# Optimization experiments

Measured on AMD Instinct MI355X. Metric: run time of the kernel, lower is better.

Reference implementation:

```python
import jax, jax.numpy as jnp
import numpy as np

E = 320000   # num edges / messages
N = 10000    # num target nodes (dim_size)
C = 256      # in_channels == out_channels


def setup_inputs() -> dict:
    key = jax.random.key(0)
    k1, k2, k3, k4, k5, k6 = jax.random.split(key, 6)
    s = 1.0 / np.sqrt(C)  # torch Linear default init bound
    return {
        "from_tensor": jax.random.normal(k1, (E, C), dtype=jnp.float32),
        "to_index": jax.random.randint(k2, (E,), 0, N),
        "dim_size": N,
        "W1": jax.random.uniform(k3, (C, C), jnp.float32, -s, s),
        "b1": jax.random.uniform(k4, (C,), jnp.float32, -s, s),
        "W2": jax.random.uniform(k5, (C, C), jnp.float32, -s, s),
        "b2": jax.random.uniform(k6, (C,), jnp.float32, -s, s),
    }


def reference(from_tensor, to_index, dim_size, W1, b1, W2, b2):
    # InterMessage with transform_scatter=True, num_layers=2, reduction='mean':
    # message = MLP(from_tensor); out = scatter_mean(message, to_index, dim_size)
    m = jax.nn.relu(from_tensor @ W1 + b1)          # [E, C]
    m = jax.nn.relu(m @ W2 + b2)                    # [E, C]
    sums = jax.ops.segment_sum(m, to_index, num_segments=dim_size)  # [N, C]
    cnt = jax.ops.segment_sum(jnp.ones((m.shape[0], 1), m.dtype), to_index,
                              num_segments=dim_size)                # [N, 1]
    # scatter-mean: empty segments produce 0 (matches torch_scatter 'mean')
    return jnp.where(cnt > 0, sums / jnp.maximum(cnt, 1.0), 0.0)
```

## Files before the change

### kernel.cpp

```cpp
#include <hip/hip_runtime.h>

#define NUM_E 320000
#define NUM_N 10000
#define PADC 32

typedef __attribute__((ext_vector_type(8))) short bf16x8;
typedef __attribute__((ext_vector_type(4))) float f32x4;

__device__ __forceinline__ short f2bf(float f) {
  unsigned u = __builtin_bit_cast(unsigned, f);
  u += 0x7FFFu + ((u >> 16) & 1u);
  return (short)(u >> 16);
}

__device__ __forceinline__ unsigned pack2bf(float x, float y) {
  unsigned ux = __builtin_bit_cast(unsigned, x);
  unsigned uy = __builtin_bit_cast(unsigned, y);
  ux += 0x7FFFu + ((ux >> 16) & 1u);
  uy += 0x7FFFu + ((uy >> 16) & 1u);
  return __builtin_amdgcn_perm(uy, ux, 0x07060302u);
}

__global__ __launch_bounds__(256) void zero_repack_k(
    const float* __restrict__ W1, const float* __restrict__ W2,
    short* __restrict__ Wp, int* __restrict__ cntA, int* __restrict__ cursor,
    float* __restrict__ out) {
  const int gtid = blockIdx.x * 256 + threadIdx.x;
  const int gsz = gridDim.x * 256;
  if (gtid == 0) *cursor = 0;
  for (int i = gtid; i < 640000; i += gsz)
    reinterpret_cast<float4*>(out)[i] = make_float4(0.f, 0.f, 0.f, 0.f);
  for (int i = gtid; i < NUM_N * PADC / 4; i += gsz)
    reinterpret_cast<int4*>(cntA)[i] = make_int4(0, 0, 0, 0);
  if (gtid < 16384) {
    const float* W = (gtid & 8192) ? W2 : W1;
    int r = gtid & 8191;
    short* dst = Wp + (gtid >> 13) * 65536 + r * 8;
    int j = r >> 9;
    int s = (r >> 6) & 7;
    int lane = r & 63;
    int n = j * 16 + (lane & 15);
    int k0 = s * 32 + (lane >> 4) * 8;
    short tmp[8];
#pragma unroll
    for (int e = 0; e < 8; ++e) tmp[e] = f2bf(W[(k0 + e) * 256 + n]);
#pragma unroll
    for (int e = 0; e < 8; ++e) dst[e] = tmp[e];
  }
}

__global__ __launch_bounds__(256) void hist_k(const int* __restrict__ idx,
                                              int* __restrict__ cntA) {
  int e = blockIdx.x * 256 + threadIdx.x;
  if (e < NUM_E) atomicAdd(&cntA[idx[e] * PADC], 1);
}

__global__ __launch_bounds__(256) void alloc_k(const int* __restrict__ cntA,
                                               int* __restrict__ fillP,
                                               float* __restrict__ inv,
                                               int* __restrict__ cursor) {
  int n = blockIdx.x * 256 + threadIdx.x;
  int lane = threadIdx.x & 63;
  int c = (n < NUM_N) ? cntA[n * PADC] : 0;
  int pre = c;
#pragma unroll
  for (int off = 1; off < 64; off <<= 1) {
    int v = __shfl_up(pre, off, 64);
    if (lane >= off) pre += v;
  }
  int tot = __shfl(pre, 63, 64);
  int base = 0;
  if (lane == 63) base = atomicAdd(cursor, tot);
  base = __shfl(base, 63, 64);
  if (n < NUM_N) {
    fillP[n * PADC] = base + pre - c;
    inv[n] = (c > 0) ? 1.0f / (float)c : 0.0f;
  }
}

__global__ __launch_bounds__(256) void scatter_k(const int* __restrict__ idx,
                                                 int* __restrict__ fillP,
                                                 int* __restrict__ sorted) {
  int e = blockIdx.x * 256 + threadIdx.x;
  if (e < NUM_E) {
    int ix = idx[e];
    int pos = atomicAdd(&fillP[ix * PADC], 1);
    sorted[pos] = e;
  }
}

__global__ __launch_bounds__(256, 3) void fused_mlp_gather(
    const float* __restrict__ X, const int* __restrict__ idx,
    const int* __restrict__ sorted,
    const short* __restrict__ Wp1, const short* __restrict__ Wp2,
    const float* __restrict__ b1, const float* __restrict__ b2,
    const float* __restrict__ inv, float* __restrict__ out) {
  __shared__ __align__(16) short Xl[64][264];
  __shared__ int idxl[64];
  __shared__ int se[64];
  __shared__ int segLo[64];
  __shared__ int segN[64];
  __shared__ int nsegS;

  const int tid = threadIdx.x;
  const int wave = tid >> 6;
  const int lane = tid & 63;
  const int q = lane >> 4;
  const int m = lane & 15;
  const int row0 = blockIdx.x * 64;

  if (tid < 64) {
    int e = sorted[row0 + tid];
    se[tid] = e;
    idxl[tid] = idx[e];
  }
  __syncthreads();

  float4 vbuf[16];
#pragma unroll
  for (int k = 0; k < 16; ++k) {
    int i = tid + k * 256;
    int r = i >> 6, c4 = i & 63;
    vbuf[k] = reinterpret_cast<const float4*>(X + (size_t)se[r] * 256)[c4];
  }
#pragma unroll
  for (int k = 0; k < 16; ++k) {
    int i = tid + k * 256;
    int r = i >> 6, c4 = i & 63;
    uint2 p;
    p.x = pack2bf(vbuf[k].x, vbuf[k].y);
    p.y = pack2bf(vbuf[k].z, vbuf[k].w);
    *reinterpret_cast<uint2*>(&Xl[r][c4 * 4]) = p;
  }
  __syncthreads();

  if (wave == 0) {
    bool flag = (lane == 0) || (idxl[lane] != idxl[lane - 1]);
    unsigned long long mask = __ballot(flag);
    if (lane == 0) nsegS = (int)__popcll(mask);
    if (flag) {
      int sidx = (int)__popcll(mask & ((1ull << lane) - 1ull));
      segLo[sidx] = lane;
      segN[sidx] = idxl[lane];
    }
  }

  f32x4 acc[4][4];
#pragma unroll
  for (int mi = 0; mi < 4; ++mi)
#pragma unroll
    for (int nj = 0; nj < 4; ++nj) acc[mi][nj] = (f32x4)0.0f;

#pragma unroll
  for (int s = 0; s < 8; ++s) {
    bf16x8 a[4], b[4];
#pragma unroll
    for (int mi = 0; mi < 4; ++mi)
      a[mi] = *reinterpret_cast<const bf16x8*>(&Xl[mi * 16 + m][s * 32 + q * 8]);
#pragma unroll
    for (int nj = 0; nj < 4; ++nj)
      b[nj] = *reinterpret_cast<const bf16x8*>(
          Wp1 + (size_t)(((wave * 4 + nj) * 8 + s) * 64 + lane) * 8);
    __builtin_amdgcn_s_setprio(1);
#pragma unroll
    for (int mi = 0; mi < 4; ++mi)
#pragma unroll
      for (int nj = 0; nj < 4; ++nj)
        acc[mi][nj] = __builtin_amdgcn_mfma_f32_16x16x32_bf16(a[mi], b[nj],
                                                              acc[mi][nj], 0, 0, 0);
    __builtin_amdgcn_s_setprio(0);
  }
  __syncthreads();

  float bias1[4];
#pragma unroll
  for (int nj = 0; nj < 4; ++nj) bias1[nj] = b1[wave * 64 + nj * 16 + m];
#pragma unroll
  for (int mi = 0; mi < 4; ++mi)
#pragma unroll
    for (int nj = 0; nj < 4; ++nj)
#pragma unroll
      for (int r4 = 0; r4 < 4; ++r4) {
        float v = fmaxf(acc[mi][nj][r4] + bias1[nj], 0.0f);
        Xl[mi * 16 + q * 4 + r4][wave * 64 + nj * 16 + m] = f2bf(v);
      }
  __syncthreads();

#pragma unroll
  for (int mi = 0; mi < 4; ++mi)
#pragma unroll
    for (int nj = 0; nj < 4; ++nj) acc[mi][nj] = (f32x4)0.0f;

#pragma unroll
  for (int s = 0; s < 8; ++s) {
    bf16x8 a[4], b[4];
#pragma unroll
    for (int mi = 0; mi < 4; ++mi)
      a[mi] = *reinterpret_cast<const bf16x8*>(&Xl[mi * 16 + m][s * 32 + q * 8]);
#pragma unroll
    for (int nj = 0; nj < 4; ++nj)
      b[nj] = *reinterpret_cast<const bf16x8*>(
          Wp2 + (size_t)(((wave * 4 + nj) * 8 + s) * 64 + lane) * 8);
    __builtin_amdgcn_s_setprio(1);
#pragma unroll
    for (int mi = 0; mi < 4; ++mi)
#pragma unroll
      for (int nj = 0; nj < 4; ++nj)
        acc[mi][nj] = __builtin_amdgcn_mfma_f32_16x16x32_bf16(a[mi], b[nj],
                                                              acc[mi][nj], 0, 0, 0);
    __builtin_amdgcn_s_setprio(0);
  }

  float bias2[4];
#pragma unroll
  for (int nj = 0; nj < 4; ++nj) bias2[nj] = b2[wave * 64 + nj * 16 + m];
#pragma unroll
  for (int mi = 0; mi < 4; ++mi)
#pragma unroll
    for (int nj = 0; nj < 4; ++nj)
#pragma unroll
      for (int r4 = 0; r4 < 4; ++r4)
        acc[mi][nj][r4] = fmaxf(acc[mi][nj][r4] + bias2[nj], 0.0f);

  int nseg = nsegS;
  for (int s = 0; s < nseg; ++s) {
    int lo = segLo[s];
    int hi = (s + 1 < nseg) ? segLo[s + 1] : 64;
    int node = segN[s];
    float sum[4] = {0.0f, 0.0f, 0.0f, 0.0f};
#pragma unroll
    for (int mi = 0; mi < 4; ++mi)
#pragma unroll
      for (int r4 = 0; r4 < 4; ++r4) {
        int row = mi * 16 + q * 4 + r4;
        float msk = (row >= lo && row < hi) ? 1.0f : 0.0f;
#pragma unroll
        for (int nj = 0; nj < 4; ++nj) sum[nj] = fmaf(msk, acc[mi][nj][r4], sum[nj]);
      }
    float scale = inv[node];
#pragma unroll
    for (int nj = 0; nj < 4; ++nj) {
      float v = sum[nj];
      v += __shfl_xor(v, 16, 64);
      v += __shfl_xor(v, 32, 64);
      if (q == 0 && v != 0.0f)
        atomicAdd(&out[(size_t)node * 256 + wave * 64 + nj * 16 + m], v * scale);
    }
  }
}

extern "C" void kernel_launch(void* const* d_in, const int* in_sizes, int n_in,
                              void* d_out, int out_size, void* d_ws, size_t ws_size,
                              hipStream_t stream) {
  const float* X   = (const float*)d_in[0];
  const int*   idx = (const int*)d_in[1];
  const float* W1  = (const float*)d_in[3];
  const float* b1  = (const float*)d_in[4];
  const float* W2  = (const float*)d_in[5];
  const float* b2  = (const float*)d_in[6];
  float* out = (float*)d_out;

  char* ws = (char*)d_ws;
  short* Wp     = (short*)(ws);
  int*   cntA   = (int*)(ws + 262144);
  int*   fillP  = (int*)(ws + 1542144);
  float* inv    = (float*)(ws + 2822144);
  int*   cursor = (int*)(ws + 2863104);
  int*   sorted = cntA;

  zero_repack_k<<<2048, 256, 0, stream>>>(W1, W2, Wp, cntA, cursor, out);
  hist_k<<<(NUM_E + 255) / 256, 256, 0, stream>>>(idx, cntA);
  alloc_k<<<40, 256, 0, stream>>>(cntA, fillP, inv, cursor);
  scatter_k<<<(NUM_E + 255) / 256, 256, 0, stream>>>(idx, fillP, sorted);
  fused_mlp_gather<<<NUM_E / 64, 256, 0, stream>>>(
      X, idx, sorted, Wp, Wp + 65536, b1, b2, inv, out);
}
```

Before: 545.3 us.

## Software-pipeline gather of next edge tile behind MLP compute in persistent blocks

```diff
diff --git a/kernel.cpp b/kernel.cpp
--- a/kernel.cpp
+++ b/kernel.cpp
@@ -89,162 +89,199 @@
   }
 }
 
-__global__ __launch_bounds__(256, 3) void fused_mlp_gather(
+__global__ __launch_bounds__(256, 2) void fused_mlp_gather(
     const float* __restrict__ X, const int* __restrict__ idx,
     const int* __restrict__ sorted,
     const short* __restrict__ Wp1, const short* __restrict__ Wp2,
     const float* __restrict__ b1, const float* __restrict__ b2,
     const float* __restrict__ inv, float* __restrict__ out) {
-  __shared__ __align__(16) short Xl[64][264];
-  __shared__ int idxl[64];
-  __shared__ int se[64];
-  __shared__ int segLo[64];
-  __shared__ int segN[64];
-  __shared__ int nsegS;
+  __shared__ __align__(16) short Xl[2][64][264];
+  __shared__ int segLo[2][64];
+  __shared__ int segN[2][64];
+  __shared__ int nsegS[2];
 
   const int tid = threadIdx.x;
   const int wave = tid >> 6;
   const int lane = tid & 63;
   const int q = lane >> 4;
   const int m = lane & 15;
-  const int row0 = blockIdx.x * 64;
-
-  if (tid < 64) {
-    int e = sorted[row0 + tid];
-    se[tid] = e;
-    idxl[tid] = idx[e];
-  }
-  __syncthreads();
+  const int row0 = blockIdx.x * 256;
+
+  float bias1v[4], bias2v[4];
+#pragma unroll
+  for (int nj = 0; nj < 4; ++nj) {
+    bias1v[nj] = b1[wave * 64 + nj * 16 + m];
+    bias2v[nj] = b2[wave * 64 + nj * 16 + m];
+  }
 
   float4 vbuf[16];
-#pragma unroll
-  for (int k = 0; k < 16; ++k) {
-    int i = tid + k * 256;
-    int r = i >> 6, c4 = i & 63;
-    vbuf[k] = reinterpret_cast<const float4*>(X + (size_t)se[r] * 256)[c4];
-  }
-#pragma unroll
-  for (int k = 0; k < 16; ++k) {
-    int i = tid + k * 256;
-    int r = i >> 6, c4 = i & 63;
-    uint2 p;
-    p.x = pack2bf(vbuf[k].x, vbuf[k].y);
-    p.y = pack2bf(vbuf[k].z, vbuf[k].w);
-    *reinterpret_cast<uint2*>(&Xl[r][c4 * 4]) = p;
-  }
-  __syncthreads();
-
-  if (wave == 0) {
-    bool flag = (lane == 0) || (idxl[lane] != idxl[lane - 1]);
-    unsigned long long mask = __ballot(flag);
-    if (lane == 0) nsegS = (int)__popcll(mask);
-    if (flag) {
-      int sidx = (int)__popcll(mask & ((1ull << lane) - 1ull));
-      segLo[sidx] = lane;
-      segN[sidx] = idxl[lane];
-    }
-  }
-
-  f32x4 acc[4][4];
-#pragma unroll
-  for (int mi = 0; mi < 4; ++mi)
-#pragma unroll
-    for (int nj = 0; nj < 4; ++nj) acc[mi][nj] = (f32x4)0.0f;
-
-#pragma unroll
-  for (int s = 0; s < 8; ++s) {
-    bf16x8 a[4], b[4];
+
+  {
+    int ew = sorted[row0 + lane];
+    if (wave == 0) {
+      int ix = idx[ew];
+      int prev = __shfl_up(ix, 1, 64);
+      bool flag = (lane == 0) || (ix != prev);
+      unsigned long long mask = __ballot(flag);
+      if (lane == 0) nsegS[0] = (int)__popcll(mask);
+      if (flag) {
+        int sidx = (int)__popcll(mask & ((1ull << lane) - 1ull));
+        segLo[0][sidx] = lane;
+        segN[0][sidx] = ix;
+      }
+    }
+#pragma unroll
+    for (int k = 0; k < 16; ++k) {
+      int e = __shfl(ew, k * 4 + wave, 64);
+      vbuf[k] = reinterpret_cast<const float4*>(X + (size_t)e * 256)[lane];
+    }
+#pragma unroll
+    for (int k = 0; k < 16; ++k) {
+      uint2 pk;
+      pk.x = pack2bf(vbuf[k].x, vbuf[k].y);
+      pk.y = pack2bf(vbuf[k].z, vbuf[k].w);
+      *reinterpret_cast<uint2*>(&Xl[0][k * 4 + wave][lane * 4]) = pk;
+    }
+  }
+
+  for (int t = 0; t < 4; ++t) {
+    const int p = t & 1;
+
+    bool sflag = false;
+    int ssidx = 0, six = 0, snseg = 0;
+    if (t < 3) {
+      int ew = sorted[row0 + (t + 1) * 64 + lane];
+      if (wave == 0) {
+        int ix = idx[ew];
+        int prev = __shfl_up(ix, 1, 64);
+        sflag = (lane == 0) || (ix != prev);
+        unsigned long long mask = __ballot(sflag);
+        snseg = (int)__popcll(mask);
+        ssidx = (int)__popcll(mask & ((1ull << lane) - 1ull));
+        six = ix;
+      }
+#pragma unroll
+      for (int k = 0; k < 16; ++k) {
+        int e = __shfl(ew, k * 4 + wave, 64);
+        vbuf[k] = reinterpret_cast<const float4*>(X + (size_t)e * 256)[lane];
+      }
+      __builtin_amdgcn_sched_barrier(0);
+    }
+    __syncthreads();
+
+    if (t < 3 && wave == 0) {
+      if (lane == 0) nsegS[1 - p] = snseg;
+      if (sflag) {
+        segLo[1 - p][ssidx] = lane;
+        segN[1 - p][ssidx] = six;
+      }
+    }
+
+    f32x4 acc[4][4];
 #pragma unroll
     for (int mi = 0; mi < 4; ++mi)
-      a[mi] = *reinterpret_cast<const bf16x8*>(&Xl[mi * 16 + m][s * 32 + q * 8]);
-#pragma unroll
-    for (int nj = 0; nj < 4; ++nj)
-      b[nj] = *reinterpret_cast<const bf16x8*>(
-          Wp1 + (size_t)(((wave * 4 + nj) * 8 + s) * 64 + lane) * 8);
-    __builtin_amdgcn_s_setprio(1);
+#pragma unroll
+      for (int nj = 0; nj < 4; ++nj) acc[mi][nj] = (f32x4)0.0f;
+
+#pragma unroll
+    for (int s = 0; s < 8; ++s) {
+      bf16x8 a[4], b[4];
+#pragma unroll
+      for (int mi = 0; mi < 4; ++mi)
+        a[mi] = *reinterpret_cast<const bf16x8*>(&Xl[p][mi * 16 + m][s * 32 + q * 8]);
+#pragma unroll
+      for (int nj = 0; nj < 4; ++nj)
+        b[nj] = *reinterpret_cast<const bf16x8*>(
+            Wp1 + (size_t)(((wave * 4 + nj) * 8 + s) * 64 + lane) * 8);
+      __builtin_amdgcn_s_setprio(1);
+#pragma unroll
+      for (int mi = 0; mi < 4; ++mi)
+#pragma unroll
+        for (int nj = 0; nj < 4; ++nj)
+          acc[mi][nj] = __builtin_amdgcn_mfma_f32_16x16x32_bf16(a[mi], b[nj],
+                                                                acc[mi][nj], 0, 0, 0);
+      __builtin_amdgcn_s_setprio(0);
+    }
+    __syncthreads();
+
 #pragma unroll
     for (int mi = 0; mi < 4; ++mi)
 #pragma unroll
       for (int nj = 0; nj < 4; ++nj)
-        acc[mi][nj] = __builtin_amdgcn_mfma_f32_16x16x32_bf16(a[mi], b[nj],
-                                                              acc[mi][nj], 0, 0, 0);
-    __builtin_amdgcn_s_setprio(0);
-  }
-  __syncthreads();
-
-  float bias1[4];
-#pragma unroll
-  for (int nj = 0; nj < 4; ++nj) bias1[nj] = b1[wave * 64 + nj * 16 + m];
-#pragma unroll
-  for (int mi = 0; mi < 4; ++mi)
-#pragma unroll
-    for (int nj = 0; nj < 4; ++nj)
-#pragma unroll
-      for (int r4 = 0; r4 < 4; ++r4) {
-        float v = fmaxf(acc[mi][nj][r4] + bias1[nj], 0.0f);
-        Xl[mi * 16 + q * 4 + r4][wave * 64 + nj * 16 + m] = f2bf(v);
-      }
-  __syncthreads();
-
-#pragma unroll
-  for (int mi = 0; mi < 4; ++mi)
-#pragma unroll
-    for (int nj = 0; nj < 4; ++nj) acc[mi][nj] = (f32x4)0.0f;
-
-#pragma unroll
-  for (int s = 0; s < 8; ++s) {
-    bf16x8 a[4], b[4];
+#pragma unroll
+        for (int r4 = 0; r4 < 4; ++r4) {
+          float v = fmaxf(acc[mi][nj][r4] + bias1v[nj], 0.0f);
+          Xl[p][mi * 16 + q * 4 + r4][wave * 64 + nj * 16 + m] = f2bf(v);
+        }
+    __syncthreads();
+
 #pragma unroll
     for (int mi = 0; mi < 4; ++mi)
-      a[mi] = *reinterpret_cast<const bf16x8*>(&Xl[mi * 16 + m][s * 32 + q * 8]);
-#pragma unroll
-    for (int nj = 0; nj < 4; ++nj)
-      b[nj] = *reinterpret_cast<const bf16x8*>(
-          Wp2 + (size_t)(((wave * 4 + nj) * 8 + s) * 64 + lane) * 8);
-    __builtin_amdgcn_s_setprio(1);
+#pragma unroll
+      for (int nj = 0; nj < 4; ++nj) acc[mi][nj] = (f32x4)0.0f;
+
+#pragma unroll
+    for (int s = 0; s < 8; ++s) {
+      bf16x8 a[4], b[4];
+#pragma unroll
+      for (int mi = 0; mi < 4; ++mi)
+        a[mi] = *reinterpret_cast<const bf16x8*>(&Xl[p][mi * 16 + m][s * 32 + q * 8]);
+#pragma unroll
+      for (int nj = 0; nj < 4; ++nj)
+        b[nj] = *reinterpret_cast<const bf16x8*>(
+            Wp2 + (size_t)(((wave * 4 + nj) * 8 + s) * 64 + lane) * 8);
+      __builtin_amdgcn_s_setprio(1);
+#pragma unroll
+      for (int mi = 0; mi < 4; ++mi)
+#pragma unroll
+        for (int nj = 0; nj < 4; ++nj)
+          acc[mi][nj] = __builtin_amdgcn_mfma_f32_16x16x32_bf16(a[mi], b[nj],
+                                                                acc[mi][nj], 0, 0, 0);
+      __builtin_amdgcn_s_setprio(0);
+    }
+
 #pragma unroll
     for (int mi = 0; mi < 4; ++mi)
 #pragma unroll
       for (int nj = 0; nj < 4; ++nj)
-        acc[mi][nj] = __builtin_amdgcn_mfma_f32_16x16x32_bf16(a[mi], b[nj],
-                                                              acc[mi][nj], 0, 0, 0);
-    __builtin_amdgcn_s_setprio(0);
-  }
-
-  float bias2[4];
-#pragma unroll
-  for (int nj = 0; nj < 4; ++nj) bias2[nj] = b2[wave * 64 + nj * 16 + m];
-#pragma unroll
-  for (int mi = 0; mi < 4; ++mi)
-#pragma unroll
-    for (int nj = 0; nj < 4; ++nj)
-#pragma unroll
-      for (int r4 = 0; r4 < 4; ++r4)
-        acc[mi][nj][r4] = fmaxf(acc[mi][nj][r4] + bias2[nj], 0.0f);
-
-  int nseg = nsegS;
-  for (int s = 0; s < nseg; ++s) {
-    int lo = segLo[s];
-    int hi = (s + 1 < nseg) ? segLo[s + 1] : 64;
-    int node = segN[s];
-    float sum[4] = {0.0f, 0.0f, 0.0f, 0.0f};
-#pragma unroll
-    for (int mi = 0; mi < 4; ++mi)
-#pragma unroll
-      for (int r4 = 0; r4 < 4; ++r4) {
-        int row = mi * 16 + q * 4 + r4;
-        float msk = (row >= lo && row < hi) ? 1.0f : 0.0f;
-#pragma unroll
-        for (int nj = 0; nj < 4; ++nj) sum[nj] = fmaf(msk, acc[mi][nj][r4], sum[nj]);
-      }
-    float scale = inv[node];
-#pragma unroll
-    for (int nj = 0; nj < 4; ++nj) {
-      float v = sum[nj];
-      v += __shfl_xor(v, 16, 64);
-      v += __shfl_xor(v, 32, 64);
-      if (q == 0 && v != 0.0f)
-        atomicAdd(&out[(size_t)node * 256 + wave * 64 + nj * 16 + m], v * scale);
+#pragma unroll
+        for (int r4 = 0; r4 < 4; ++r4)
+          acc[mi][nj][r4] = fmaxf(acc[mi][nj][r4] + bias2v[nj], 0.0f);
+
+    int nseg = nsegS[p];
+    for (int s = 0; s < nseg; ++s) {
+      int lo = segLo[p][s];
+      int hi = (s + 1 < nseg) ? segLo[p][s + 1] : 64;
+      int node = segN[p][s];
+      float sum[4] = {0.0f, 0.0f, 0.0f, 0.0f};
+#pragma unroll
+      for (int mi = 0; mi < 4; ++mi)
+#pragma unroll
+        for (int r4 = 0; r4 < 4; ++r4) {
+          int row = mi * 16 + q * 4 + r4;
+          float msk = (row >= lo && row < hi) ? 1.0f : 0.0f;
+#pragma unroll
+          for (int nj = 0; nj < 4; ++nj) sum[nj] = fmaf(msk, acc[mi][nj][r4], sum[nj]);
+        }
+      float scale = inv[node];
+#pragma unroll
+      for (int nj = 0; nj < 4; ++nj) {
+        float v = sum[nj];
+        v += __shfl_xor(v, 16, 64);
+        v += __shfl_xor(v, 32, 64);
+        if (q == 0 && v != 0.0f)
+          atomicAdd(&out[(size_t)node * 256 + wave * 64 + nj * 16 + m], v * scale);
+      }
+    }
+
+    if (t < 3) {
+#pragma unroll
+      for (int k = 0; k < 16; ++k) {
+        uint2 pk;
+        pk.x = pack2bf(vbuf[k].x, vbuf[k].y);
+        pk.y = pack2bf(vbuf[k].z, vbuf[k].w);
+        *reinterpret_cast<uint2*>(&Xl[1 - p][k * 4 + wave][lane * 4]) = pk;
+      }
     }
   }
 }
@@ -272,6 +309,6 @@
   hist_k<<<(NUM_E + 255) / 256, 256, 0, stream>>>(idx, cntA);
   alloc_k<<<40, 256, 0, stream>>>(cntA, fillP, inv, cursor);
   scatter_k<<<(NUM_E + 255) / 256, 256, 0, stream>>>(idx, fillP, sorted);
-  fused_mlp_gather<<<NUM_E / 64, 256, 0, stream>>>(
+  fused_mlp_gather<<<NUM_E / 256, 256, 0, stream>>>(
       X, idx, sorted, Wp, Wp + 65536, b1, b2, inv, out);
 }
```

Measured after the change: 750.3 us. +37.6%, slower.
